# Performance work log

Measured on AMD Instinct MI355X. Metric: run time of the kernel, lower is better.

Reference implementation:

```python
import jax, jax.numpy as jnp
import numpy as np
from jax.scipy.linalg import expm

N_QUBITS = 13
N_LAYERS = 4  # ceil(log2(13))


def _apply_2axes(T, M, a0, a1):
    """Apply 4x4 matrix M to the pair of 2-dim axes (a0, a1) of tensor T."""
    nd = T.ndim
    T = jnp.moveaxis(T, (a0, a1), (nd - 2, nd - 1))
    s = T.shape
    T = (T.reshape(s[:-2] + (4,)) @ M.T).reshape(s)
    return jnp.moveaxis(T, (nd - 2, nd - 1), (a0, a1))


def _conv_pairs(n):
    pairs = [(2 * i, 2 * i + 1) for i in range(n // 2)]
    if n > 2:
        pairs += [(2 * i + 1, (2 * i + 2) % n) for i in range(n // 2)]
    return pairs


def _conv_state(psi, U, n):
    # psi: [B] + [2]*n pure state
    for q0, q1 in _conv_pairs(n):
        psi = _apply_2axes(psi, U, 1 + q0, 1 + q1)
    return psi


def _conv_dm(rho, U, n):
    # rho: [B] + [2]*n (rows) + [2]*n (cols); apply U on rows, U* on cols
    Uc = U.conj()
    for q0, q1 in _conv_pairs(n):
        rho = _apply_2axes(rho, U, 1 + q0, 1 + q1)
        rho = _apply_2axes(rho, Uc, 1 + n + q0, 1 + n + q1)
    return rho


def _pool_dm(rho, n):
    # measure-and-discard qubits 0..n//2-1 (with index shifting these are the
    # original even-indexed qubits); averaging over outcomes == partial trace.
    measured = [2 * i for i in range(n // 2)]
    cur = n
    for q in reversed(measured):  # descending so lower indices stay valid
        rho = jnp.trace(rho, axis1=1 + q, axis2=1 + cur + q)
        cur -= 1
    return rho, cur


def setup_inputs() -> dict:
    key = jax.random.key(0)
    k1, k2, k3, k4 = jax.random.split(key, 4)
    B, D = 2, 2 ** N_QUBITS
    return {
        "psi_real": jax.random.normal(k1, (B, D), dtype=jnp.float32),
        "psi_imag": jax.random.normal(k2, (B, D), dtype=jnp.float32),
        "H_real": jax.random.normal(k3, (N_LAYERS, 4, 4), dtype=jnp.float32),
        "H_imag": jax.random.normal(k4, (N_LAYERS, 4, 4), dtype=jnp.float32),
    }


def reference(psi_real, psi_imag, H_real, H_imag):
    B = psi_real.shape[0]
    n = N_QUBITS
    psi = (psi_real + 1j * psi_imag).astype(jnp.complex64)
    psi = psi / jnp.linalg.norm(psi, axis=1, keepdims=True)
    H = (H_real + 1j * H_imag).astype(jnp.complex64)
    # anti-hermitian generator -> unitary gate per layer
    Us = [expm(H[i] - H[i].conj().T) for i in range(N_LAYERS)]

    # layer 0: conv on pure state, then convert to density matrix, then pool
    psi = psi.reshape((B,) + (2,) * n)
    psi = _conv_state(psi, Us[0], n)
    flat = psi.reshape(B, -1)
    rho = (flat[:, :, None] * flat[:, None, :].conj()).reshape((B,) + (2,) * (2 * n))
    rho, n = _pool_dm(rho, n)

    for i in range(1, N_LAYERS):
        rho = _conv_dm(rho, Us[i], n)
        rho, n = _pool_dm(rho, n)

    # n == 1 here: measure qubit 0, return P(outcome 0)
    rho = rho.reshape(B, 2, 2)
    return rho[:, 0, 0].real
```

## Files before the change

kernel.cpp:

```cpp
#include <hip/hip_runtime.h>


#define NT 256
#define DIM 8192

typedef float v2f __attribute__((ext_vector_type(2)));

__device__ __forceinline__ float2 cadds(float2 a, float2 b) {
    return make_float2(a.x + b.x, a.y + b.y);
}
__device__ __forceinline__ float2 cmacs(float2 acc, float2 a, float2 b) {
    acc.x = fmaf(a.x, b.x, fmaf(-a.y, b.y, acc.x));
    acc.y = fmaf(a.x, b.y, fmaf(a.y, b.x, acc.y));
    return acc;
}
__device__ __forceinline__ float2 shflc(float2 v, int src) {
    return make_float2(__shfl(v.x, src, 64), __shfl(v.y, src, 64));
}

__device__ __forceinline__ v2f cma(v2f acc, v2f u, v2f us, v2f a) {
#pragma clang fp contract(fast)
    v2f ax = __builtin_shufflevector(a, a, 0, 0);
    v2f ay = __builtin_shufflevector(a, a, 1, 1);
    acc = ax * u + acc;
    acc = ay * us + acc;
    return acc;
}

__device__ float2 expm_compute(float are, float aim) {
    const int lane = threadIdx.x & 63;
    const int e = lane & 15, r = e >> 2, c = e & 3;
    const int base = lane & 48;

    float v = fabsf(are) + fabsf(aim);
    v += __shfl_xor(v, 1, 64);
    v += __shfl_xor(v, 2, 64);
    v = fmaxf(v, __shfl_xor(v, 4, 64));
    v = fmaxf(v, __shfl_xor(v, 8, 64));
    v = fmaxf(v, __shfl_xor(v, 16, 64));
    v = fmaxf(v, __shfl_xor(v, 32, 64));

    int s = 0;
    while (v > 0.25f && s < 30) { v *= 0.5f; s++; }
    const float scale = ldexpf(1.0f, -s);

    float2 X = make_float2(are * scale, aim * scale);
    float2 E = X;
    if (r == c) E.x += 1.0f;
    float2 T = X;
    for (int k = 2; k <= 10; k++) {
        float2 acc = make_float2(0.f, 0.f);
        #pragma unroll
        for (int kk = 0; kk < 4; kk++) {
            float2 t = shflc(T, base + r * 4 + kk);
            float2 x = shflc(X, base + kk * 4 + c);
            acc = cmacs(acc, t, x);
        }
        const float inv = 1.0f / (float)k;
        T = make_float2(acc.x * inv, acc.y * inv);
        E = cadds(E, T);
    }
    for (int i = 0; i < s; i++) {
        float2 acc = make_float2(0.f, 0.f);
        #pragma unroll
        for (int kk = 0; kk < 4; kk++) {
            float2 a = shflc(E, base + r * 4 + kk);
            float2 bb = shflc(E, base + kk * 4 + c);
            acc = cmacs(acc, a, bb);
        }
        E = acc;
    }
    return E;
}

__device__ __forceinline__ void loadU(float2 E, int L, v2f* u, v2f* us) {
    #pragma unroll
    for (int k = 0; k < 16; k++) {
        float ur = __shfl(E.x, (L << 4) | k, 64);
        float ui = __shfl(E.y, (L << 4) | k, 64);
        u[k] = (v2f){ur, ui};
        us[k] = (v2f){-ui, ur};
    }
}

__device__ __forceinline__ int swz(int e) {
    return e ^ ((e >> 3) & 14) ^ ((e >> 7) & 15) ^ ((e >> 10) & 14);
}

template<int MASK>
__device__ __forceinline__ int deposit(int t) {
    int r = 0;
    #pragma unroll
    for (int p = 0; p < 13; p++) {
        if (MASK & (1 << p)) { r |= (t & 1) << p; t >>= 1; }
    }
    return r;
}

template<int B4, int B3, int B2, int B1, int B0>
__device__ __forceinline__ int eaddr5(int base, int i) {
    return base | (((i >> 4) & 1) << B4) | (((i >> 3) & 1) << B3)
                | (((i >> 2) & 1) << B2) | (((i >> 1) & 1) << B1)
                | ((i & 1) << B0);
}

template<int B4, int B3, int B2, int B1, int B0, int MASK>
__device__ __forceinline__ void phase_read(v2f* v, const v2f* psi, int t) {
    const int base = deposit<MASK>(t);
    #pragma unroll
    for (int i = 0; i < 32; i++) v[i] = psi[swz(eaddr5<B4, B3, B2, B1, B0>(base, i))];
}
template<int B4, int B3, int B2, int B1, int B0, int MASK>
__device__ __forceinline__ void phase_write(const v2f* v, v2f* psi, int t) {
    const int base = deposit<MASK>(t);
    #pragma unroll
    for (int i = 0; i < 32; i++) psi[swz(eaddr5<B4, B3, B2, B1, B0>(base, i))] = v[i];
}

template<int KA, int KB>
__device__ __forceinline__ void apply_gate(v2f* v, const v2f* u, const v2f* us) {
    const int MA = 1 << KA, MB = 1 << KB;
    #pragma unroll
    for (int i = 0; i < 32; i++) {
        if (i & (MA | MB)) continue;
        v2f a0 = v[i], a1 = v[i | MB], a2 = v[i | MA], a3 = v[i | MA | MB];
        v2f z = {0.f, 0.f};
        v2f n0 = cma(cma(cma(cma(z, u[0], us[0], a0), u[1], us[1], a1),
                         u[2], us[2], a2), u[3], us[3], a3);
        v2f n1 = cma(cma(cma(cma(z, u[4], us[4], a0), u[5], us[5], a1),
                         u[6], us[6], a2), u[7], us[7], a3);
        v2f n2 = cma(cma(cma(cma(z, u[8], us[8], a0), u[9], us[9], a1),
                         u[10], us[10], a2), u[11], us[11], a3);
        v2f n3 = cma(cma(cma(cma(z, u[12], us[12], a0), u[13], us[13], a1),
                         u[14], us[14], a2), u[15], us[15], a3);
        v[i] = n0; v[i | MB] = n1; v[i | MA] = n2; v[i | MA | MB] = n3;
    }
}

__global__ __launch_bounds__(NT, 1) void qcnn_kernel(
    const float* __restrict__ pr, const float* __restrict__ pi,
    const float* __restrict__ Hr, const float* __restrict__ Hi,
    float* __restrict__ out) {
    __shared__ v2f psi[DIM];
    const int t = threadIdx.x;
    const int b = blockIdx.x;
    const int lane = t & 63;
    const int m = lane >> 4, ee = lane & 15, r = ee >> 2, c = ee & 3;

    float hra = Hr[m * 16 + r * 4 + c], hrb = Hr[m * 16 + c * 4 + r];
    float hia = Hi[m * 16 + r * 4 + c], hib = Hi[m * 16 + c * 4 + r];

    const float* prb = pr + b * DIM;
    const float* pib = pi + b * DIM;
    v2f v[32];
    #pragma unroll
    for (int i = 0; i < 32; i++)
        v[i] = (v2f){prb[t | (i << 8)], pib[t | (i << 8)]};

    float2 E = expm_compute(hra - hrb, hia + hib);

    float norm2 = 0.f;
    #pragma unroll
    for (int i = 0; i < 32; i++)
        norm2 = fmaf(v[i].x, v[i].x, fmaf(v[i].y, v[i].y, norm2));

    v2f u[16], us[16];
    loadU(E, 0, u, us);

    apply_gate<4, 3>(v, u, us);
    apply_gate<2, 1>(v, u, us);
    apply_gate<3, 2>(v, u, us);
    phase_write<12, 11, 10, 9, 8, 0x00FF>(v, psi, t);
    __syncthreads();

    phase_read<8, 7, 6, 5, 4, 0x1E0F>(v, psi, t);
    apply_gate<4, 3>(v, u, us);
    apply_gate<2, 1>(v, u, us);
    apply_gate<3, 2>(v, u, us);
    phase_write<8, 7, 6, 5, 4, 0x1E0F>(v, psi, t);
    __syncthreads();

    phase_read<4, 3, 2, 1, 0, 0x1FE0>(v, psi, t);
    apply_gate<4, 3>(v, u, us);
    apply_gate<2, 1>(v, u, us);
    apply_gate<3, 2>(v, u, us);
    apply_gate<1, 0>(v, u, us);
    loadU(E, 1, u, us);
    apply_gate<3, 1>(v, u, us);
    apply_gate<1, 0>(v, u, us);
    loadU(E, 2, u, us);
    apply_gate<1, 0>(v, u, us);
    phase_write<4, 3, 2, 1, 0, 0x1FE0>(v, psi, t);
    __syncthreads();

    phase_read<9, 8, 7, 5, 4, 0x1C4F>(v, psi, t);
    loadU(E, 0, u, us);
    apply_gate<4, 3>(v, u, us);
    apply_gate<1, 0>(v, u, us);
    loadU(E, 1, u, us);
    apply_gate<2, 1>(v, u, us);
    phase_write<9, 8, 7, 5, 4, 0x1C4F>(v, psi, t);
    __syncthreads();

    phase_read<11, 9, 7, 5, 3, 0x1557>(v, psi, t);
    apply_gate<4, 3>(v, u, us);
    apply_gate<3, 2>(v, u, us);
    apply_gate<1, 0>(v, u, us);
    loadU(E, 2, u, us);
    apply_gate<3, 1>(v, u, us);
    phase_write<11, 9, 7, 5, 3, 0x1557>(v, psi, t);
    __syncthreads();

    phase_read<12, 9, 5, 1, 0, 0x0DDC>(v, psi, t);
    apply_gate<2, 1>(v, u, us);
    apply_gate<0, 3>(v, u, us);
    loadU(E, 3, u, us);
    apply_gate<2, 0>(v, u, us);

    float s0 = 0.f;
    #pragma unroll
    for (int i = 0; i < 32; i += 2)
        s0 = fmaf(v[i].x, v[i].x, fmaf(v[i].y, v[i].y, s0));

    #pragma unroll
    for (int off = 1; off < 64; off <<= 1) {
        s0 += __shfl_xor(s0, off, 64);
        norm2 += __shfl_xor(norm2, off, 64);
    }
    __syncthreads();
    if (lane == 0) psi[t >> 6] = (v2f){s0, norm2};
    __syncthreads();
    if (t == 0) {
        float S = 0.f, Nrm = 0.f;
        #pragma unroll
        for (int w = 0; w < NT / 64; w++) { S += psi[w].x; Nrm += psi[w].y; }
        out[b] = S / Nrm;
    }
}

extern "C" void kernel_launch(void* const* d_in, const int* in_sizes, int n_in,
                              void* d_out, int out_size, void* d_ws, size_t ws_size,
                              hipStream_t stream) {
    const float* pr = (const float*)d_in[0];
    const float* pi = (const float*)d_in[1];
    const float* Hr = (const float*)d_in[2];
    const float* Hi = (const float*)d_in[3];
    float* out = (float*)d_out;
    qcnn_kernel<<<dim3(out_size), dim3(NT), 0, stream>>>(pr, pi, Hr, Hi, out);
}
```

Baseline: 82.47 us.

## Split each batch state across two blocks by the top qubit after first gate

Each batch element is now handled by two workgroups. Both apply the first gate on the highest qubit pair, and each keeps one half of the 13-qubit state, which is possible because that qubit is traced out and the two halves never mix afterwards. Per-thread register arrays and shared memory are halved, and all later phases are rescheduled over 12 qubits. The two partial probabilities are combined with an atomicAdd after a memset, which adds an extra launch and requires exact normalization by the full norm in each half.

```diff
diff --git a/kernel.cpp b/kernel.cpp
--- a/kernel.cpp
+++ b/kernel.cpp
@@ -2,7 +2,7 @@
 
 
 #define NT 256
-#define DIM 8192
+#define HDIM 4096
 
 typedef float v2f __attribute__((ext_vector_type(2)));
 
@@ -84,44 +84,43 @@
 }
 
 __device__ __forceinline__ int swz(int e) {
-    return e ^ ((e >> 3) & 14) ^ ((e >> 7) & 15) ^ ((e >> 10) & 14);
+    return e ^ ((e >> 4) & 15) ^ ((e >> 8) & 15);
 }
 
 template<int MASK>
 __device__ __forceinline__ int deposit(int t) {
     int r = 0;
     #pragma unroll
-    for (int p = 0; p < 13; p++) {
+    for (int p = 0; p < 12; p++) {
         if (MASK & (1 << p)) { r |= (t & 1) << p; t >>= 1; }
     }
     return r;
 }
 
-template<int B4, int B3, int B2, int B1, int B0>
-__device__ __forceinline__ int eaddr5(int base, int i) {
-    return base | (((i >> 4) & 1) << B4) | (((i >> 3) & 1) << B3)
-                | (((i >> 2) & 1) << B2) | (((i >> 1) & 1) << B1)
-                | ((i & 1) << B0);
-}
-
-template<int B4, int B3, int B2, int B1, int B0, int MASK>
+template<int B3, int B2, int B1, int B0>
+__device__ __forceinline__ int eaddr4(int base, int i) {
+    return base | (((i >> 3) & 1) << B3) | (((i >> 2) & 1) << B2)
+                | (((i >> 1) & 1) << B1) | ((i & 1) << B0);
+}
+
+template<int B3, int B2, int B1, int B0, int MASK>
 __device__ __forceinline__ void phase_read(v2f* v, const v2f* psi, int t) {
     const int base = deposit<MASK>(t);
     #pragma unroll
-    for (int i = 0; i < 32; i++) v[i] = psi[swz(eaddr5<B4, B3, B2, B1, B0>(base, i))];
-}
-template<int B4, int B3, int B2, int B1, int B0, int MASK>
+    for (int i = 0; i < 16; i++) v[i] = psi[swz(eaddr4<B3, B2, B1, B0>(base, i))];
+}
+template<int B3, int B2, int B1, int B0, int MASK>
 __device__ __forceinline__ void phase_write(const v2f* v, v2f* psi, int t) {
     const int base = deposit<MASK>(t);
     #pragma unroll
-    for (int i = 0; i < 32; i++) psi[swz(eaddr5<B4, B3, B2, B1, B0>(base, i))] = v[i];
+    for (int i = 0; i < 16; i++) psi[swz(eaddr4<B3, B2, B1, B0>(base, i))] = v[i];
 }
 
 template<int KA, int KB>
 __device__ __forceinline__ void apply_gate(v2f* v, const v2f* u, const v2f* us) {
     const int MA = 1 << KA, MB = 1 << KB;
     #pragma unroll
-    for (int i = 0; i < 32; i++) {
+    for (int i = 0; i < 16; i++) {
         if (i & (MA | MB)) continue;
         v2f a0 = v[i], a1 = v[i | MB], a2 = v[i | MA], a3 = v[i | MA | MB];
         v2f z = {0.f, 0.f};
@@ -141,77 +140,105 @@
     const float* __restrict__ pr, const float* __restrict__ pi,
     const float* __restrict__ Hr, const float* __restrict__ Hi,
     float* __restrict__ out) {
-    __shared__ v2f psi[DIM];
+    __shared__ v2f psi[HDIM];
     const int t = threadIdx.x;
-    const int b = blockIdx.x;
+    const int b = blockIdx.x >> 1;
+    const int h = blockIdx.x & 1;
     const int lane = t & 63;
     const int m = lane >> 4, ee = lane & 15, r = ee >> 2, c = ee & 3;
 
     float hra = Hr[m * 16 + r * 4 + c], hrb = Hr[m * 16 + c * 4 + r];
     float hia = Hi[m * 16 + r * 4 + c], hib = Hi[m * 16 + c * 4 + r];
 
-    const float* prb = pr + b * DIM;
-    const float* pib = pi + b * DIM;
-    v2f v[32];
+    const float* prb = pr + b * 2 * HDIM;
+    const float* pib = pi + b * 2 * HDIM;
+    v2f w[32];
+    #pragma unroll
+    for (int i = 0; i < 32; i++) {
+        int g = (((i >> 4) & 1) << 12) | (((i >> 3) & 1) << 11)
+              | (((i >> 2) & 1) << 10) | (((i >> 1) & 1) << 9)
+              | ((i & 1) << 8) | t;
+        w[i] = (v2f){prb[g], pib[g]};
+    }
+
+    float2 E = expm_compute(hra - hrb, hia + hib);
+
+    float norm2 = 0.f;
     #pragma unroll
     for (int i = 0; i < 32; i++)
-        v[i] = (v2f){prb[t | (i << 8)], pib[t | (i << 8)]};
-
-    float2 E = expm_compute(hra - hrb, hia + hib);
-
-    float norm2 = 0.f;
-    #pragma unroll
-    for (int i = 0; i < 32; i++)
-        norm2 = fmaf(v[i].x, v[i].x, fmaf(v[i].y, v[i].y, norm2));
+        norm2 = fmaf(w[i].x, w[i].x, fmaf(w[i].y, w[i].y, norm2));
 
     v2f u[16], us[16];
     loadU(E, 0, u, us);
 
-    apply_gate<4, 3>(v, u, us);
-    apply_gate<2, 1>(v, u, us);
-    apply_gate<3, 2>(v, u, us);
-    phase_write<12, 11, 10, 9, 8, 0x00FF>(v, psi, t);
-    __syncthreads();
-
-    phase_read<8, 7, 6, 5, 4, 0x1E0F>(v, psi, t);
-    apply_gate<4, 3>(v, u, us);
-    apply_gate<2, 1>(v, u, us);
-    apply_gate<3, 2>(v, u, us);
-    phase_write<8, 7, 6, 5, 4, 0x1E0F>(v, psi, t);
-    __syncthreads();
-
-    phase_read<4, 3, 2, 1, 0, 0x1FE0>(v, psi, t);
-    apply_gate<4, 3>(v, u, us);
-    apply_gate<2, 1>(v, u, us);
-    apply_gate<3, 2>(v, u, us);
+    v2f v[16];
+    #pragma unroll
+    for (int i = 0; i < 8; i++) {
+        v2f a0 = w[i], a1 = w[i | 8], a2 = w[i | 16], a3 = w[i | 24];
+        v2f z = {0.f, 0.f};
+        v2f lo, hi;
+        if (h == 0) {
+            lo = cma(cma(cma(cma(z, u[0], us[0], a0), u[1], us[1], a1),
+                         u[2], us[2], a2), u[3], us[3], a3);
+            hi = cma(cma(cma(cma(z, u[4], us[4], a0), u[5], us[5], a1),
+                         u[6], us[6], a2), u[7], us[7], a3);
+        } else {
+            lo = cma(cma(cma(cma(z, u[8], us[8], a0), u[9], us[9], a1),
+                         u[10], us[10], a2), u[11], us[11], a3);
+            hi = cma(cma(cma(cma(z, u[12], us[12], a0), u[13], us[13], a1),
+                         u[14], us[14], a2), u[15], us[15], a3);
+        }
+        v[i] = lo; v[i | 8] = hi;
+    }
+    apply_gate<2, 1>(v, u, us);
+    apply_gate<3, 2>(v, u, us);
+    phase_write<11, 10, 9, 8, 0x0FF>(v, psi, t);
+    __syncthreads();
+
+    phase_read<8, 7, 6, 5, 0xE1F>(v, psi, t);
+    apply_gate<3, 2>(v, u, us);
+    apply_gate<1, 0>(v, u, us);
+    apply_gate<2, 1>(v, u, us);
+    phase_write<8, 7, 6, 5, 0xE1F>(v, psi, t);
+    __syncthreads();
+
+    phase_read<4, 3, 2, 1, 0xFE1>(v, psi, t);
+    apply_gate<3, 2>(v, u, us);
+    apply_gate<1, 0>(v, u, us);
+    apply_gate<2, 1>(v, u, us);
+    phase_write<4, 3, 2, 1, 0xFE1>(v, psi, t);
+    __syncthreads();
+
+    phase_read<9, 8, 5, 4, 0xCCF>(v, psi, t);
+    apply_gate<3, 2>(v, u, us);
+    apply_gate<1, 0>(v, u, us);
+    phase_write<9, 8, 5, 4, 0xCCF>(v, psi, t);
+    __syncthreads();
+
+    phase_read<11, 9, 1, 0, 0x5FC>(v, psi, t);
     apply_gate<1, 0>(v, u, us);
     loadU(E, 1, u, us);
-    apply_gate<3, 1>(v, u, us);
+    apply_gate<3, 2>(v, u, us);
+    phase_write<11, 9, 1, 0, 0x5FC>(v, psi, t);
+    __syncthreads();
+
+    phase_read<7, 5, 3, 1, 0xF55>(v, psi, t);
+    apply_gate<3, 2>(v, u, us);
+    apply_gate<1, 0>(v, u, us);
+    apply_gate<2, 1>(v, u, us);
+    phase_write<7, 5, 3, 1, 0xF55>(v, psi, t);
+    __syncthreads();
+
+    phase_read<9, 7, 1, 0, 0xD7C>(v, psi, t);
+    apply_gate<3, 2>(v, u, us);
     apply_gate<1, 0>(v, u, us);
     loadU(E, 2, u, us);
     apply_gate<1, 0>(v, u, us);
-    phase_write<4, 3, 2, 1, 0, 0x1FE0>(v, psi, t);
-    __syncthreads();
-
-    phase_read<9, 8, 7, 5, 4, 0x1C4F>(v, psi, t);
-    loadU(E, 0, u, us);
-    apply_gate<4, 3>(v, u, us);
-    apply_gate<1, 0>(v, u, us);
-    loadU(E, 1, u, us);
-    apply_gate<2, 1>(v, u, us);
-    phase_write<9, 8, 7, 5, 4, 0x1C4F>(v, psi, t);
-    __syncthreads();
-
-    phase_read<11, 9, 7, 5, 3, 0x1557>(v, psi, t);
-    apply_gate<4, 3>(v, u, us);
-    apply_gate<3, 2>(v, u, us);
-    apply_gate<1, 0>(v, u, us);
-    loadU(E, 2, u, us);
-    apply_gate<3, 1>(v, u, us);
-    phase_write<11, 9, 7, 5, 3, 0x1557>(v, psi, t);
-    __syncthreads();
-
-    phase_read<12, 9, 5, 1, 0, 0x0DDC>(v, psi, t);
+    phase_write<9, 7, 1, 0, 0xD7C>(v, psi, t);
+    __syncthreads();
+
+    phase_read<9, 5, 1, 0, 0xDDC>(v, psi, t);
+    apply_gate<3, 2>(v, u, us);
     apply_gate<2, 1>(v, u, us);
     apply_gate<0, 3>(v, u, us);
     loadU(E, 3, u, us);
@@ -219,7 +246,7 @@
 
     float s0 = 0.f;
     #pragma unroll
-    for (int i = 0; i < 32; i += 2)
+    for (int i = 0; i < 16; i += 2)
         s0 = fmaf(v[i].x, v[i].x, fmaf(v[i].y, v[i].y, s0));
 
     #pragma unroll
@@ -233,8 +260,8 @@
     if (t == 0) {
         float S = 0.f, Nrm = 0.f;
         #pragma unroll
-        for (int w = 0; w < NT / 64; w++) { S += psi[w].x; Nrm += psi[w].y; }
-        out[b] = S / Nrm;
+        for (int wv = 0; wv < NT / 64; wv++) { S += psi[wv].x; Nrm += psi[wv].y; }
+        atomicAdd(&out[b], S / Nrm);
     }
 }
 
@@ -246,5 +273,6 @@
     const float* Hr = (const float*)d_in[2];
     const float* Hi = (const float*)d_in[3];
     float* out = (float*)d_out;
-    qcnn_kernel<<<dim3(out_size), dim3(NT), 0, stream>>>(pr, pi, Hr, Hi, out);
-}
+    hipMemsetAsync(out, 0, out_size * sizeof(float), stream);
+    qcnn_kernel<<<dim3(out_size * 2), dim3(NT), 0, stream>>>(pr, pi, Hr, Hi, out);
+}
```

New measurement: 72.92 us. -11.6%, faster.
